# Kernel optimization log

Hardware: AMD Instinct MI355X
Metric: run time of the kernel (lower is better)

## Reference

```python
import jax, jax.numpy as jnp
import numpy as np

N = 16384          # points in the (single-batch) cloud
K = 16             # boundary_k
C = 20             # num semantic classes (ScanNet-style)
IGNORE = -1        # ignore_index
BOUNDARY_W = 1.0   # boundary_loss_weight


def setup_inputs() -> dict:
    key = jax.random.key(0)
    k1, k2, k3 = jax.random.split(key, 3)
    coord = jax.random.normal(k1, (N, 3), jnp.float32)
    seg_logits = jax.random.normal(k2, (N, C), jnp.float32)
    segment = jax.random.randint(k3, (N,), 0, C, dtype=jnp.int32)
    return {"coord": coord, "seg_logits": seg_logits, "segment": segment, "offset": N}


def _knn_idx(coord):
    # brute-force kNN (loop=False): exclude self via +inf diagonal
    d2 = jnp.sum(coord * coord, axis=1)                       # [N]
    dist = d2[:, None] + d2[None, :] - 2.0 * (coord @ coord.T)  # [N, N]
    dist = dist + jnp.where(jnp.eye(dist.shape[0], dtype=bool), jnp.inf, 0.0)
    _, idx = jax.lax.top_k(-dist, K)                          # [N, K] neighbor (src) indices per center (dst)
    return idx


def _masked_ce(logp_tgt, mask):
    # mean cross-entropy over masked points (matches torch reduction='mean' w/ ignore_index)
    cnt = jnp.sum(mask)
    s = jnp.sum(jnp.where(mask, logp_tgt, 0.0))
    return jnp.where(cnt > 0, -s / jnp.maximum(cnt, 1).astype(logp_tgt.dtype), 0.0)


def reference(coord, seg_logits, segment, offset):
    # --- boundary mask: knn_graph -> per-edge label diff -> scatter-max to dst ---
    nbr = _knn_idx(coord)                                     # [N, K] src indices, dst = row index
    nbr_seg = segment[nbr]                                    # gather: [N, K]
    valid_pt = segment != IGNORE                              # [N]
    valid = (nbr_seg != IGNORE) & valid_pt[:, None]           # per-edge valid
    diff = valid & (nbr_seg != segment[:, None])              # per-edge label mismatch
    boundary = jnp.any(diff, axis=1)                          # scatter-max over dst == row-wise any

    # --- main loss: cross-entropy with ignore_index ---
    logp = jax.nn.log_softmax(seg_logits, axis=-1)            # [N, C]
    tgt = jnp.clip(segment, 0, C - 1)
    logp_tgt = jnp.take_along_axis(logp, tgt[:, None], axis=1)[:, 0]  # [N]
    main_loss = _masked_ce(logp_tgt, valid_pt)

    # --- boundary loss: CE restricted to boundary points (0 if none) ---
    bmask = boundary & valid_pt
    boundary_loss = _masked_ce(logp_tgt, bmask)

    loss = main_loss + BOUNDARY_W * boundary_loss
    return loss
```

## Files before the change

kernel.cpp:

```cpp
#include <hip/hip_runtime.h>
#include <hip/hip_bf16.h>
#include <math.h>

#define N_PTS 16384
#define KNN   16
#define NCLS  20
#define BND_W 1.0f

#define THREADS 512
#define WAVES   8
#define FR      4
#define RPW     (16 * FR)
#define RPB     (WAVES * RPW)
#define RBLKS   (N_PTS / RPB)
#define CSPLIT  16
#define CAND_PB (N_PTS / CSPLIT)

typedef short  short8 __attribute__((ext_vector_type(8)));
typedef float  f32x4  __attribute__((ext_vector_type(4)));

__device__ __forceinline__ unsigned short f2bf(float x) {
    union { __hip_bfloat16 h; unsigned short u; } cv;
    cv.h = __float2bfloat16(x);
    return cv.u;
}
__device__ __forceinline__ float bf2f(unsigned short b) {
    union { __hip_bfloat16 h; unsigned short u; } cv;
    cv.u = b;
    return __bfloat162float(cv.h);
}

__device__ __forceinline__ void build_b(const float* __restrict__ coord,
                                        const int* __restrict__ seg, int j,
                                        unsigned short* out) {
    float x = coord[3 * j], y = coord[3 * j + 1], z = coord[3 * j + 2];
    int lab = seg[j];
    unsigned short xh = f2bf(x), yh = f2bf(y), zh = f2bf(z);
    unsigned short xl = f2bf(x - bf2f(xh));
    unsigned short yl = f2bf(y - bf2f(yh));
    unsigned short zl = f2bf(z - bf2f(zh));
    float h = 0.5f * fmaf(x, x, fmaf(y, y, z * z));
    unsigned short hh = f2bf(h);
    unsigned short hl = f2bf(h - bf2f(hh));
    out[0] = xh; out[1] = xh; out[2] = xl;
    out[3] = yh; out[4] = yh; out[5] = yl;
    out[6] = zh; out[7] = zh; out[8] = zl;
    out[9]  = hh ^ 0x8000u;
    out[10] = hl ^ 0x8000u;
#pragma unroll
    for (int s = 0; s < NCLS; s++) out[11 + s] = (lab == s) ? 0x3F80u : 0u;
    out[31] = (lab < 0) ? 0x3F80u : 0u;
}

template<bool PASS1>
__device__ __forceinline__ short8 build_a_frag(const float* __restrict__ coord,
                                               const int* __restrict__ seg,
                                               int row, int g) {
    __attribute__((aligned(16))) unsigned short s[8];
    const unsigned short one = 0x3F80u;
    const unsigned short nb = PASS1 ? 0xC480u : 0u;
    if (g == 0) {
        float x = coord[3 * row], y = coord[3 * row + 1], z = coord[3 * row + 2];
        unsigned short xh = f2bf(x), yh = f2bf(y), zh = f2bf(z);
        s[0] = xh; s[1] = f2bf(x - bf2f(xh)); s[2] = xh;
        s[3] = yh; s[4] = f2bf(y - bf2f(yh)); s[5] = yh;
        s[6] = zh; s[7] = f2bf(z - bf2f(zh));
    } else if (g == 1) {
        float z = coord[3 * row + 2];
        int lab = seg[row];
        s[0] = f2bf(z); s[1] = one; s[2] = one;
        s[3] = (lab == 0) ? nb : 0u; s[4] = (lab == 1) ? nb : 0u;
        s[5] = (lab == 2) ? nb : 0u; s[6] = (lab == 3) ? nb : 0u;
        s[7] = (lab == 4) ? nb : 0u;
    } else if (g == 2) {
        int lab = seg[row];
        s[0] = (lab == 5) ? nb : 0u;  s[1] = (lab == 6) ? nb : 0u;
        s[2] = (lab == 7) ? nb : 0u;  s[3] = (lab == 8) ? nb : 0u;
        s[4] = (lab == 9) ? nb : 0u;  s[5] = (lab == 10) ? nb : 0u;
        s[6] = (lab == 11) ? nb : 0u; s[7] = (lab == 12) ? nb : 0u;
    } else {
        int lab = seg[row];
        s[0] = (lab == 13) ? nb : 0u; s[1] = (lab == 14) ? nb : 0u;
        s[2] = (lab == 15) ? nb : 0u; s[3] = (lab == 16) ? nb : 0u;
        s[4] = (lab == 17) ? nb : 0u; s[5] = (lab == 18) ? nb : 0u;
        s[6] = (lab == 19) ? nb : 0u; s[7] = nb;
    }
    return *(const short8*)s;
}

__device__ __forceinline__ float waveReduceSum(float v) {
#pragma unroll
    for (int off = 32; off > 0; off >>= 1) v += __shfl_down(v, off, 64);
    return v;
}

template<bool PASS1>
__global__ __launch_bounds__(THREADS, 4) void k_pass(
    const float* __restrict__ coord, const int* __restrict__ seg,
    const float* __restrict__ logits,
    float* __restrict__ smax_part, int* __restrict__ cnt,
    float* __restrict__ accum, int* __restrict__ done_rb,
    unsigned* __restrict__ done_final, float* __restrict__ out)
{
    __shared__ __align__(16) unsigned short bsm[CAND_PB * 32];
    __shared__ float thr_lds[RPB];
    __shared__ int s_flag;
    const int tid  = threadIdx.x;
    const int lane = tid & 63, wave = tid >> 6;
    const int l15  = lane & 15, l4 = lane >> 4;
    const int rb   = blockIdx.x * RPB;
    const int split = blockIdx.y;
    const int cb   = split * CAND_PB;

    if (PASS1 && split == 0) {
        cnt[rb + tid] = 0;
        if (tid == 5) done_rb[blockIdx.x] = 0;
        if (blockIdx.x == 0) {
            if (tid < 4) accum[tid] = 0.f;
            if (tid == 4) *done_final = 0u;
        }
    }

    {
        __attribute__((aligned(16))) unsigned short be[32];
        short8* wp = (short8*)bsm;
#pragma unroll
        for (int u = 0; u < 2; u++) {
            int c = 2 * tid + u;
            build_b(coord, seg, cb + c, be);
            int swz = (c >> 1) & 3;
#pragma unroll
            for (int kb = 0; kb < 4; kb++)
                wp[c * 4 + (kb ^ swz)] = ((const short8*)be)[kb];
        }
    }

    short8 af[FR];
#pragma unroll
    for (int f = 0; f < FR; f++)
        af[f] = build_a_frag<PASS1>(coord, seg, rb + wave * RPW + f * 16 + l15, l4);

    if (!PASS1) {
        int row = rb + tid;
        float m = smax_part[row];
#pragma unroll
        for (int s = 1; s < CSPLIT; s++) m = fmaxf(m, smax_part[s * N_PTS + row]);
        thr_lds[tid] = m;
    }
    __syncthreads();

    float thr[FR][4];
    if (!PASS1) {
#pragma unroll
        for (int f = 0; f < FR; f++)
#pragma unroll
            for (int r = 0; r < 4; r++)
                thr[f][r] = thr_lds[wave * RPW + f * 16 + l4 * 4 + r];
    }

    f32x4 rmax[FR];
    int cv[FR][4];
#pragma unroll
    for (int f = 0; f < FR; f++)
#pragma unroll
        for (int r = 0; r < 4; r++) { rmax[f][r] = -3.0e38f; cv[f][r] = 0; }

    const short8* bp = (const short8*)bsm;
    const int bidx = l15 * 4 + (l4 ^ ((l15 >> 1) & 3));
    const f32x4 zero = {0.f, 0.f, 0.f, 0.f};

#pragma unroll 2
    for (int c0 = 0; c0 < CAND_PB; c0 += 32) {
        short8 bA = bp[bidx + c0 * 4];
        short8 bB = bp[bidx + (c0 + 16) * 4];
        f32x4 dA[FR], dB[FR];
#pragma unroll
        for (int f = 0; f < FR; f++)
            dA[f] = __builtin_amdgcn_mfma_f32_16x16x32_bf16(af[f], bA, zero, 0, 0, 0);
#pragma unroll
        for (int f = 0; f < FR; f++)
            dB[f] = __builtin_amdgcn_mfma_f32_16x16x32_bf16(af[f], bB, zero, 0, 0, 0);
        if (PASS1) {
#pragma unroll
            for (int f = 0; f < FR; f++)
#pragma unroll
                for (int r = 0; r < 4; r++)
                    rmax[f][r] = fmaxf(fmaxf(rmax[f][r], dA[f][r]), dB[f][r]);
        } else {
#pragma unroll
            for (int f = 0; f < FR; f++)
#pragma unroll
                for (int r = 0; r < 4; r++)
                    cv[f][r] += ((dA[f][r] > thr[f][r]) ? 1 : 0)
                              + ((dB[f][r] > thr[f][r]) ? 1 : 0);
        }
    }

    if (PASS1) {
#pragma unroll
        for (int m = 1; m < 16; m <<= 1)
#pragma unroll
            for (int f = 0; f < FR; f++)
#pragma unroll
                for (int r = 0; r < 4; r++)
                    rmax[f][r] = fmaxf(rmax[f][r], __shfl_xor(rmax[f][r], m, 64));
        if (l15 == 0) {
#pragma unroll
            for (int f = 0; f < FR; f++)
#pragma unroll
                for (int r = 0; r < 4; r++)
                    smax_part[split * N_PTS + rb + wave * RPW + f * 16 + l4 * 4 + r] = rmax[f][r];
        }
    } else {
#pragma unroll
        for (int m = 1; m < 16; m <<= 1)
#pragma unroll
            for (int f = 0; f < FR; f++)
#pragma unroll
                for (int r = 0; r < 4; r++)
                    cv[f][r] += __shfl_xor(cv[f][r], m, 64);
        if (l15 == 0) {
#pragma unroll
            for (int f = 0; f < FR; f++)
#pragma unroll
                for (int r = 0; r < 4; r++)
                    atomicAdd(&cnt[rb + wave * RPW + f * 16 + l4 * 4 + r], cv[f][r]);
        }

        __syncthreads();
        if (tid == 0) {
            __threadfence();
            s_flag = (atomicAdd(&done_rb[blockIdx.x], 1) == CSPLIT - 1) ? 1 : 0;
        }
        __syncthreads();
        if (s_flag) {
            const int row = rb + tid;
            int sg = seg[row];
            bool valid = (sg != -1);
            const float4* row4 = (const float4*)(logits + (size_t)row * NCLS);
            float a[NCLS];
            float4 v0 = row4[0], v1 = row4[1], v2 = row4[2], v3 = row4[3], v4 = row4[4];
            a[0]=v0.x; a[1]=v0.y; a[2]=v0.z; a[3]=v0.w;
            a[4]=v1.x; a[5]=v1.y; a[6]=v1.z; a[7]=v1.w;
            a[8]=v2.x; a[9]=v2.y; a[10]=v2.z; a[11]=v2.w;
            a[12]=v3.x; a[13]=v3.y; a[14]=v3.z; a[15]=v3.w;
            a[16]=v4.x; a[17]=v4.y; a[18]=v4.z; a[19]=v4.w;
            float mx = a[0];
#pragma unroll
            for (int c = 1; c < NCLS; c++) mx = fmaxf(mx, a[c]);
            float se = 0.f;
#pragma unroll
            for (int c = 0; c < NCLS; c++) se += __expf(a[c] - mx);
            int tgt = min(max(sg, 0), NCLS - 1);
            float at = 0.f;
#pragma unroll
            for (int c = 0; c < NCLS; c++) at += (c == tgt) ? a[c] : 0.f;
            float logp = at - mx - __logf(se);
            int crow = atomicAdd(&cnt[row], 0);
            bool bnd = valid && ((crow - 1) < KNN);
            float sm = valid ? logp : 0.f, nm = valid ? 1.f : 0.f;
            float sb = bnd ? logp : 0.f,  nb2 = bnd ? 1.f : 0.f;
            sm = waveReduceSum(sm); nm = waveReduceSum(nm);
            sb = waveReduceSum(sb); nb2 = waveReduceSum(nb2);
            if ((tid & 63) == 0) {
                atomicAdd(&accum[0], sm);
                atomicAdd(&accum[1], nm);
                atomicAdd(&accum[2], sb);
                atomicAdd(&accum[3], nb2);
            }
            __syncthreads();
            if (tid == 0) {
                __threadfence();
                if (atomicAdd(done_final, 1u) == (unsigned)(RBLKS - 1)) {
                    float Sm = atomicAdd(&accum[0], 0.f);
                    float Cm = atomicAdd(&accum[1], 0.f);
                    float Sb = atomicAdd(&accum[2], 0.f);
                    float Cb = atomicAdd(&accum[3], 0.f);
                    float main_loss = (Cm > 0.f) ? (-Sm / fmaxf(Cm, 1.f)) : 0.f;
                    float bnd_loss  = (Cb > 0.f) ? (-Sb / fmaxf(Cb, 1.f)) : 0.f;
                    out[0] = main_loss + BND_W * bnd_loss;
                }
            }
        }
    }
}

extern "C" void kernel_launch(void* const* d_in, const int* in_sizes, int n_in,
                              void* d_out, int out_size, void* d_ws, size_t ws_size,
                              hipStream_t stream) {
    const float* coord  = (const float*)d_in[0];
    const float* logits = (const float*)d_in[1];
    const int*   seg    = (const int*)d_in[2];
    (void)in_sizes; (void)n_in; (void)out_size; (void)ws_size;

    float*    smax_part = (float*)d_ws;
    int*      cnt       = (int*)((char*)d_ws + CSPLIT * N_PTS * 4);
    char*     tail      = (char*)d_ws + CSPLIT * N_PTS * 4 + N_PTS * 4;
    float*    accum     = (float*)tail;
    int*      done_rb   = (int*)(tail + 16);
    unsigned* done_final= (unsigned*)(tail + 16 + RBLKS * 4);

    dim3 grid(RBLKS, CSPLIT);
    k_pass<true> <<<grid, THREADS, 0, stream>>>(coord, seg, logits, smax_part, cnt,
                                                accum, done_rb, done_final, (float*)d_out);
    k_pass<false><<<grid, THREADS, 0, stream>>>(coord, seg, logits, smax_part, cnt,
                                                accum, done_rb, done_final, (float*)d_out);
}
```

Before: 64.02 us.

## Precompute bf16 point encodings in a separate kernel and stream B from global

Adds a pre-pass kernel that encodes every point once into A and B bf16 fragment layouts in workspace and does the counter/accumulator initialization. The two kNN passes then load A fragments directly and read B fragments from global/L2 each iteration instead of building them into LDS per block. This removes the redundant per-block encoding work and the LDS staging with its barrier. In exchange it adds a kernel launch, and the inner loop now depends on global-memory loads that go through cache rather than LDS.

```diff
diff --git a/kernel.cpp b/kernel.cpp
--- a/kernel.cpp
+++ b/kernel.cpp
@@ -30,11 +30,17 @@
     return __bfloat162float(cv.h);
 }
 
-__device__ __forceinline__ void build_b(const float* __restrict__ coord,
-                                        const int* __restrict__ seg, int j,
-                                        unsigned short* out) {
-    float x = coord[3 * j], y = coord[3 * j + 1], z = coord[3 * j + 2];
-    int lab = seg[j];
+__global__ __launch_bounds__(256) void k_enc(const float* __restrict__ coord,
+                                             const int* __restrict__ seg,
+                                             unsigned short* __restrict__ aenc,
+                                             unsigned short* __restrict__ benc,
+                                             int* __restrict__ cnt,
+                                             float* __restrict__ accum,
+                                             int* __restrict__ done_rb,
+                                             unsigned* __restrict__ done_final) {
+    const int i = blockIdx.x * 256 + threadIdx.x;
+    float x = coord[3 * i], y = coord[3 * i + 1], z = coord[3 * i + 2];
+    int lab = seg[i];
     unsigned short xh = f2bf(x), yh = f2bf(y), zh = f2bf(z);
     unsigned short xl = f2bf(x - bf2f(xh));
     unsigned short yl = f2bf(y - bf2f(yh));
@@ -42,50 +48,38 @@
     float h = 0.5f * fmaf(x, x, fmaf(y, y, z * z));
     unsigned short hh = f2bf(h);
     unsigned short hl = f2bf(h - bf2f(hh));
-    out[0] = xh; out[1] = xh; out[2] = xl;
-    out[3] = yh; out[4] = yh; out[5] = yl;
-    out[6] = zh; out[7] = zh; out[8] = zl;
-    out[9]  = hh ^ 0x8000u;
-    out[10] = hl ^ 0x8000u;
-#pragma unroll
-    for (int s = 0; s < NCLS; s++) out[11 + s] = (lab == s) ? 0x3F80u : 0u;
-    out[31] = (lab < 0) ? 0x3F80u : 0u;
-}
-
-template<bool PASS1>
-__device__ __forceinline__ short8 build_a_frag(const float* __restrict__ coord,
-                                               const int* __restrict__ seg,
-                                               int row, int g) {
-    __attribute__((aligned(16))) unsigned short s[8];
-    const unsigned short one = 0x3F80u;
-    const unsigned short nb = PASS1 ? 0xC480u : 0u;
-    if (g == 0) {
-        float x = coord[3 * row], y = coord[3 * row + 1], z = coord[3 * row + 2];
-        unsigned short xh = f2bf(x), yh = f2bf(y), zh = f2bf(z);
-        s[0] = xh; s[1] = f2bf(x - bf2f(xh)); s[2] = xh;
-        s[3] = yh; s[4] = f2bf(y - bf2f(yh)); s[5] = yh;
-        s[6] = zh; s[7] = f2bf(z - bf2f(zh));
-    } else if (g == 1) {
-        float z = coord[3 * row + 2];
-        int lab = seg[row];
-        s[0] = f2bf(z); s[1] = one; s[2] = one;
-        s[3] = (lab == 0) ? nb : 0u; s[4] = (lab == 1) ? nb : 0u;
-        s[5] = (lab == 2) ? nb : 0u; s[6] = (lab == 3) ? nb : 0u;
-        s[7] = (lab == 4) ? nb : 0u;
-    } else if (g == 2) {
-        int lab = seg[row];
-        s[0] = (lab == 5) ? nb : 0u;  s[1] = (lab == 6) ? nb : 0u;
-        s[2] = (lab == 7) ? nb : 0u;  s[3] = (lab == 8) ? nb : 0u;
-        s[4] = (lab == 9) ? nb : 0u;  s[5] = (lab == 10) ? nb : 0u;
-        s[6] = (lab == 11) ? nb : 0u; s[7] = (lab == 12) ? nb : 0u;
-    } else {
-        int lab = seg[row];
-        s[0] = (lab == 13) ? nb : 0u; s[1] = (lab == 14) ? nb : 0u;
-        s[2] = (lab == 15) ? nb : 0u; s[3] = (lab == 16) ? nb : 0u;
-        s[4] = (lab == 17) ? nb : 0u; s[5] = (lab == 18) ? nb : 0u;
-        s[6] = (lab == 19) ? nb : 0u; s[7] = nb;
-    }
-    return *(const short8*)s;
+    const unsigned short one = 0x3F80u, nb = 0xC480u;
+
+    __attribute__((aligned(16))) unsigned short a[32], b[32];
+    a[0] = xh; a[1] = xl; a[2] = xh;
+    a[3] = yh; a[4] = yl; a[5] = yh;
+    a[6] = zh; a[7] = zl; a[8] = zh;
+    a[9] = one; a[10] = one;
+#pragma unroll
+    for (int s = 0; s < NCLS; s++) a[11 + s] = (lab == s) ? nb : 0u;
+    a[31] = nb;
+
+    b[0] = xh; b[1] = xh; b[2] = xl;
+    b[3] = yh; b[4] = yh; b[5] = yl;
+    b[6] = zh; b[7] = zh; b[8] = zl;
+    b[9]  = hh ^ 0x8000u;
+    b[10] = hl ^ 0x8000u;
+#pragma unroll
+    for (int s = 0; s < NCLS; s++) b[11 + s] = (lab == s) ? one : 0u;
+    b[31] = (lab < 0) ? one : 0u;
+
+    short8* ap = (short8*)(aenc + (size_t)i * 32);
+    short8* bp = (short8*)(benc + (size_t)i * 32);
+#pragma unroll
+    for (int kb = 0; kb < 4; kb++) {
+        ap[kb] = ((const short8*)a)[kb];
+        bp[kb] = ((const short8*)b)[kb];
+    }
+
+    cnt[i] = 0;
+    if (i < 4) accum[i] = 0.f;
+    if (i == 4) *done_final = 0u;
+    if (i >= 8 && i < 8 + RBLKS) done_rb[i - 8] = 0;
 }
 
 __device__ __forceinline__ float waveReduceSum(float v) {
@@ -96,13 +90,13 @@
 
 template<bool PASS1>
 __global__ __launch_bounds__(THREADS, 4) void k_pass(
-    const float* __restrict__ coord, const int* __restrict__ seg,
-    const float* __restrict__ logits,
+    const unsigned short* __restrict__ aenc,
+    const unsigned short* __restrict__ benc,
+    const int* __restrict__ seg, const float* __restrict__ logits,
     float* __restrict__ smax_part, int* __restrict__ cnt,
     float* __restrict__ accum, int* __restrict__ done_rb,
     unsigned* __restrict__ done_final, float* __restrict__ out)
 {
-    __shared__ __align__(16) unsigned short bsm[CAND_PB * 32];
     __shared__ float thr_lds[RPB];
     __shared__ int s_flag;
     const int tid  = threadIdx.x;
@@ -112,45 +106,29 @@
     const int split = blockIdx.y;
     const int cb   = split * CAND_PB;
 
-    if (PASS1 && split == 0) {
-        cnt[rb + tid] = 0;
-        if (tid == 5) done_rb[blockIdx.x] = 0;
-        if (blockIdx.x == 0) {
-            if (tid < 4) accum[tid] = 0.f;
-            if (tid == 4) *done_final = 0u;
-        }
-    }
-
-    {
-        __attribute__((aligned(16))) unsigned short be[32];
-        short8* wp = (short8*)bsm;
-#pragma unroll
-        for (int u = 0; u < 2; u++) {
-            int c = 2 * tid + u;
-            build_b(coord, seg, cb + c, be);
-            int swz = (c >> 1) & 3;
-#pragma unroll
-            for (int kb = 0; kb < 4; kb++)
-                wp[c * 4 + (kb ^ swz)] = ((const short8*)be)[kb];
-        }
-    }
-
     short8 af[FR];
 #pragma unroll
     for (int f = 0; f < FR; f++)
-        af[f] = build_a_frag<PASS1>(coord, seg, rb + wave * RPW + f * 16 + l15, l4);
-
+        af[f] = *(const short8*)(aenc + (size_t)(rb + wave * RPW + f * 16 + l15) * 32 + l4 * 8);
+    if (!PASS1) {
+#pragma unroll
+        for (int f = 0; f < FR; f++) {
+            union { short8 s; unsigned u[4]; } cv_;
+            cv_.s = af[f];
+            if (l4 == 1) { cv_.u[1] &= 0x0000FFFFu; cv_.u[2] = 0u; cv_.u[3] = 0u; }
+            else if (l4 >= 2) { cv_.u[0] = 0u; cv_.u[1] = 0u; cv_.u[2] = 0u; cv_.u[3] = 0u; }
+            af[f] = cv_.s;
+        }
+    }
+
+    float thr[FR][4];
     if (!PASS1) {
         int row = rb + tid;
         float m = smax_part[row];
 #pragma unroll
         for (int s = 1; s < CSPLIT; s++) m = fmaxf(m, smax_part[s * N_PTS + row]);
         thr_lds[tid] = m;
-    }
-    __syncthreads();
-
-    float thr[FR][4];
-    if (!PASS1) {
+        __syncthreads();
 #pragma unroll
         for (int f = 0; f < FR; f++)
 #pragma unroll
@@ -165,34 +143,27 @@
 #pragma unroll
         for (int r = 0; r < 4; r++) { rmax[f][r] = -3.0e38f; cv[f][r] = 0; }
 
-    const short8* bp = (const short8*)bsm;
-    const int bidx = l15 * 4 + (l4 ^ ((l15 >> 1) & 3));
+    const short8* bp = (const short8*)benc;
     const f32x4 zero = {0.f, 0.f, 0.f, 0.f};
-
-#pragma unroll 2
-    for (int c0 = 0; c0 < CAND_PB; c0 += 32) {
-        short8 bA = bp[bidx + c0 * 4];
-        short8 bB = bp[bidx + (c0 + 16) * 4];
-        f32x4 dA[FR], dB[FR];
+#pragma unroll 4
+    for (int c0 = 0; c0 < CAND_PB; c0 += 16) {
+        short8 bf = bp[(size_t)(cb + c0 + l15) * 4 + l4];
+        f32x4 d[FR];
 #pragma unroll
         for (int f = 0; f < FR; f++)
-            dA[f] = __builtin_amdgcn_mfma_f32_16x16x32_bf16(af[f], bA, zero, 0, 0, 0);
-#pragma unroll
-        for (int f = 0; f < FR; f++)
-            dB[f] = __builtin_amdgcn_mfma_f32_16x16x32_bf16(af[f], bB, zero, 0, 0, 0);
+            d[f] = __builtin_amdgcn_mfma_f32_16x16x32_bf16(af[f], bf, zero, 0, 0, 0);
         if (PASS1) {
 #pragma unroll
             for (int f = 0; f < FR; f++)
 #pragma unroll
                 for (int r = 0; r < 4; r++)
-                    rmax[f][r] = fmaxf(fmaxf(rmax[f][r], dA[f][r]), dB[f][r]);
+                    rmax[f][r] = fmaxf(rmax[f][r], d[f][r]);
         } else {
 #pragma unroll
             for (int f = 0; f < FR; f++)
 #pragma unroll
                 for (int r = 0; r < 4; r++)
-                    cv[f][r] += ((dA[f][r] > thr[f][r]) ? 1 : 0)
-                              + ((dB[f][r] > thr[f][r]) ? 1 : 0);
+                    cv[f][r] += (d[f][r] > thr[f][r]) ? 1 : 0;
         }
     }
 
@@ -293,16 +264,20 @@
     const int*   seg    = (const int*)d_in[2];
     (void)in_sizes; (void)n_in; (void)out_size; (void)ws_size;
 
-    float*    smax_part = (float*)d_ws;
-    int*      cnt       = (int*)((char*)d_ws + CSPLIT * N_PTS * 4);
-    char*     tail      = (char*)d_ws + CSPLIT * N_PTS * 4 + N_PTS * 4;
-    float*    accum     = (float*)tail;
-    int*      done_rb   = (int*)(tail + 16);
-    unsigned* done_final= (unsigned*)(tail + 16 + RBLKS * 4);
+    unsigned short* aenc = (unsigned short*)d_ws;
+    unsigned short* benc = (unsigned short*)((char*)d_ws + (1u << 20));
+    float* smax_part = (float*)((char*)d_ws + (2u << 20));
+    int*   cnt       = (int*)((char*)d_ws + (3u << 20));
+    char*  tail      = (char*)d_ws + (3u << 20) + N_PTS * 4;
+    float*    accum      = (float*)tail;
+    unsigned* done_final = (unsigned*)(tail + 16);
+    int*      done_rb    = (int*)(tail + 32);
 
     dim3 grid(RBLKS, CSPLIT);
-    k_pass<true> <<<grid, THREADS, 0, stream>>>(coord, seg, logits, smax_part, cnt,
+    k_enc        <<<N_PTS / 256, 256, 0, stream>>>(coord, seg, aenc, benc, cnt,
+                                                   accum, done_rb, done_final);
+    k_pass<true> <<<grid, THREADS, 0, stream>>>(aenc, benc, seg, logits, smax_part, cnt,
                                                 accum, done_rb, done_final, (float*)d_out);
-    k_pass<false><<<grid, THREADS, 0, stream>>>(coord, seg, logits, smax_part, cnt,
+    k_pass<false><<<grid, THREADS, 0, stream>>>(aenc, benc, seg, logits, smax_part, cnt,
                                                 accum, done_rb, done_final, (float*)d_out);
 }
```

New measurement: 78.43 us. +22.5%, slower.
